# Kernel tuning notes

Measured on AMD Instinct MI355X. Metric: run time of the kernel, lower is better.

The kernel has to match this reference:

```python
import jax, jax.numpy as jnp
import numpy as np

B, N, QD, D, S, H, K = 4, 1024, 320, 512, 1024, 8, 32
DH = D // H  # 64
EPS = 1e-5


def setup_inputs() -> dict:
    key = jax.random.key(0)
    ks = jax.random.split(key, 10)
    sc = 1.0 / np.sqrt(D)
    return {
        "query_states": jax.random.normal(ks[0], (B, N, QD), dtype=jnp.float32),
        "Wqp": jax.random.normal(ks[1], (D, QD), dtype=jnp.float32) / np.sqrt(QD),
        "mem_keys": jax.random.normal(ks[2], (S, D), dtype=jnp.float32),
        "mem_values": jax.random.normal(ks[3], (S, D), dtype=jnp.float32) * 0.1,
        "Wq": jax.random.normal(ks[4], (D, D), dtype=jnp.float32) * sc,
        "Wk": jax.random.normal(ks[5], (D, D), dtype=jnp.float32) * sc,
        "Wv": jax.random.normal(ks[6], (D, D), dtype=jnp.float32) * sc,
        "Wo": jax.random.normal(ks[7], (D, D), dtype=jnp.float32) * sc,
        "ln_g": jnp.ones((D,), dtype=jnp.float32),
        "ln_b": jnp.zeros((D,), dtype=jnp.float32),
        "Wout": jax.random.normal(ks[8], (QD, D), dtype=jnp.float32) * sc,
        "bout": jnp.zeros((QD,), dtype=jnp.float32),
    }


def _l2norm(x):
    return x / jnp.sqrt(jnp.sum(x * x, axis=-1, keepdims=True) + 1e-12)


def reference(query_states, Wqp, mem_keys, mem_values, Wq, Wk, Wv, Wo, ln_g, ln_b, Wout, bout):
    # project queries into memory space: [B,N,D]
    q = jnp.einsum("bnq,dq->bnd", query_states, Wqp)
    # normalize memory slots (normalize_slots=True)
    keys = _l2norm(mem_keys)    # [S,D]
    vals = _l2norm(mem_values)  # [S,D]
    # top-k memory-slot preselection over raw query-key scores
    scores = jnp.einsum("bnd,sd->bns", q, keys)          # [B,N,S]
    _, top_idx = jax.lax.top_k(scores, K)                  # [B,N,K]
    sel_k = jnp.take(keys, top_idx, axis=0)                # [B,N,K,D]
    sel_v = jnp.take(vals, top_idx, axis=0)                # [B,N,K,D]
    # multi-head cross-attention over gathered slots
    qh = jnp.einsum("bnd,ed->bne", q, Wq).reshape(B, N, H, DH)
    kh = jnp.einsum("bnkd,ed->bnke", sel_k, Wk).reshape(B, N, K, H, DH)
    vh = jnp.einsum("bnkd,ed->bnke", sel_v, Wv).reshape(B, N, K, H, DH)
    att = jnp.einsum("bnhd,bnkhd->bnhk", qh, kh) / jnp.sqrt(jnp.float32(DH))  # temperature=1.0
    w = jax.nn.softmax(att, axis=-1)                       # [B,N,H,K]
    ctx = jnp.einsum("bnhk,bnkhd->bnhd", w, vh).reshape(B, N, D)
    ctx = jnp.einsum("bnd,ed->bne", ctx, Wo)               # [B,N,D]
    # output projector: LayerNorm + Linear(memory_dim -> query_dim); dropout inactive (eval)
    mu = jnp.mean(ctx, axis=-1, keepdims=True)
    var = jnp.mean((ctx - mu) ** 2, axis=-1, keepdims=True)
    normed = (ctx - mu) / jnp.sqrt(var + EPS) * ln_g + ln_b
    out = jnp.einsum("bnd,qd->bnq", normed, Wout) + bout   # [B,N,QD]
    return out
```

## Files before the change

kernel.cpp:

```cpp
#include <hip/hip_runtime.h>


__device__ __forceinline__ float bf2f(unsigned short u) {
    return __uint_as_float(((unsigned int)u) << 16);
}
__device__ __forceinline__ unsigned short f2bf(float f) {
    unsigned int u = __float_as_uint(f);
    u += 0x7FFFu + ((u >> 16) & 1u);
    return (unsigned short)(u >> 16);
}
__device__ __forceinline__ int detect_bf(const void* g) {
    return ((*(const unsigned int*)g) & 0xFFFFu) != 0u;
}
__device__ __forceinline__ float ldg1(const void* p, size_t i, int bf) {
    return bf ? bf2f(((const unsigned short*)p)[i]) : ((const float*)p)[i];
}
__device__ __forceinline__ void ld4(const void* p, size_t i, int bf, float* o) {
    if (bf) {
        ushort4 v = *reinterpret_cast<const ushort4*>((const unsigned short*)p + i);
        o[0] = bf2f(v.x); o[1] = bf2f(v.y); o[2] = bf2f(v.z); o[3] = bf2f(v.w);
    } else {
        float4 v = *reinterpret_cast<const float4*>((const float*)p + i);
        o[0] = v.x; o[1] = v.y; o[2] = v.z; o[3] = v.w;
    }
}
__device__ __forceinline__ unsigned int fkey(float x) {
    unsigned int u = __float_as_uint(x);
    return (u & 0x80000000u) ? ~u : (u | 0x80000000u);
}
__device__ __forceinline__ float funkey(unsigned int k) {
    unsigned int u = (k & 0x80000000u) ? (k & 0x7FFFFFFFu) : ~k;
    return __uint_as_float(u);
}

typedef __attribute__((ext_vector_type(8))) short bf16x8;
typedef __attribute__((ext_vector_type(4))) float f32x4;
typedef __attribute__((ext_vector_type(4))) unsigned int u32x4;

__device__ __forceinline__ void split8(const float* x, u32x4& h, u32x4& l) {
#pragma unroll
    for (int j = 0; j < 4; j++) {
        float x0 = x[2 * j], x1 = x[2 * j + 1];
        unsigned int hp, lp;
        asm("v_cvt_pk_bf16_f32 %0, %1, %2" : "=v"(hp) : "v"(x0), "v"(x1));
        float h0 = __uint_as_float(hp << 16);
        float h1 = __uint_as_float(hp & 0xFFFF0000u);
        float l0 = x0 - h0, l1 = x1 - h1;
        asm("v_cvt_pk_bf16_f32 %0, %1, %2" : "=v"(lp) : "v"(l0), "v"(l1));
        h[j] = hp; l[j] = lp;
    }
}

__global__ __launch_bounds__(256) void norms_kernel(
    const void* __restrict__ keys, const void* __restrict__ vals,
    const void* __restrict__ gdet,
    float* __restrict__ inv_kf, float* __restrict__ inv_vf)
{
    __shared__ double red[256];
    int bf = detect_bf(gdet);
    int r = blockIdx.x, t = threadIdx.x;
    const void* src = (r < 1024) ? keys : vals;
    size_t base = (size_t)((r < 1024) ? r : r - 1024) * 512;
    float x0 = ldg1(src, base + t, bf), x1 = ldg1(src, base + t + 256, bf);
    red[t] = (double)x0 * x0 + (double)x1 * x1;
    __syncthreads();
    for (int s = 128; s > 0; s >>= 1) {
        if (t < s) red[t] += red[t + s];
        __syncthreads();
    }
    if (t == 0) {
        float rs = (float)(1.0 / sqrt(red[0] + 1e-12));
        if (r < 1024) inv_kf[r] = rs;
        else          inv_vf[r - 1024] = rs;
    }
}

__global__ __launch_bounds__(256) void transpose_wqp(
    const void* __restrict__ Wqp, const void* __restrict__ gdet,
    float* __restrict__ WqpT)
{
    __shared__ float tile[32][36];
    const int bf = detect_bf(gdet);
    const int t = threadIdx.x;
    const int d0 = blockIdx.x * 32, q0 = blockIdx.y * 32;
    const int r = t >> 3, c = (t & 7) * 4;
    float v[4];
    ld4(Wqp, (size_t)(d0 + r) * 320 + q0 + c, bf, v);
#pragma unroll
    for (int i = 0; i < 4; i++) tile[r][c + i] = v[i];
    __syncthreads();
    float o[4];
#pragma unroll
    for (int i = 0; i < 4; i++) o[i] = tile[c + i][r];
    *reinterpret_cast<float4*>(&WqpT[(size_t)(q0 + r) * 512 + d0 + c]) =
        make_float4(o[0], o[1], o[2], o[3]);
}

__global__ __launch_bounds__(256) void mfma_abt(
    const void* __restrict__ A, const void* __restrict__ B,
    const float* __restrict__ scale, float* __restrict__ C,
    const void* __restrict__ A2, const void* __restrict__ B2,
    const float* __restrict__ scale2, float* __restrict__ C2, int ysplit,
    const float2* __restrict__ stats, const void* __restrict__ g,
    const void* __restrict__ bvec, const void* __restrict__ bias,
    void* __restrict__ O,
    int N, int amode, int abfon, int bbfon, int epi, int npass,
    const void* __restrict__ gdet)
{
    __shared__ __align__(16) short lds[16384];
    const int AHo = 0, ALo = 4096, BHo = 8192, BLo = 12288;
    const int flag = detect_bf(gdet);
    const int abf = abfon ? flag : 0;
    const int bbf = bbfon ? flag : 0;
    const int t = threadIdx.x;
    int by = blockIdx.y;
    const void* Ap = A; const void* Bp = B;
    const float* scp = scale; float* Cp = C;
    if (ysplit && by >= ysplit) { Ap = A2; Bp = B2; scp = scale2; Cp = C2; by -= ysplit; }
    const int m0 = by * 64, n0 = blockIdx.x * 64;
    const int lane = t & 63, wv = t >> 6;
    const int wm = wv >> 1, wn = wv & 1;
    const int srow = t >> 3;
    const int sc8  = t & 7;

    int aoff[2][2], boff[2][2];
#pragma unroll
    for (int mi = 0; mi < 2; mi++)
#pragma unroll
        for (int kk = 0; kk < 2; kk++) {
            int ra = wm * 32 + mi * 16 + (lane & 15);
            int ca = kk * 4 + (lane >> 4);
            aoff[mi][kk] = ra * 64 + ((ca ^ (ra & 7)) << 3);
        }
#pragma unroll
    for (int ni = 0; ni < 2; ni++)
#pragma unroll
        for (int kk = 0; kk < 2; kk++) {
            int rb = wn * 32 + ni * 16 + (lane & 15);
            int cb = kk * 4 + (lane >> 4);
            boff[ni][kk] = rb * 64 + ((cb ^ (rb & 7)) << 3);
        }

    const int addr0 = srow * 64 + ((sc8 ^ (srow & 7)) << 3);
    const int addr1 = addr0 + 32 * 64;

    f32x4 acc[2][2];
#pragma unroll
    for (int mi = 0; mi < 2; mi++)
#pragma unroll
        for (int ni = 0; ni < 2; ni++)
            acc[mi][ni] = (f32x4){0.f, 0.f, 0.f, 0.f};

    for (int ks = 0; ks < 8; ks++) {
        const int kb = ks * 64;
        float av0[8], av1[8], bv0[8], bv1[8];
        ld4(Ap, (size_t)(m0 + srow) * 512 + kb + sc8 * 8,          abf, av0);
        ld4(Ap, (size_t)(m0 + srow) * 512 + kb + sc8 * 8 + 4,      abf, av0 + 4);
        ld4(Ap, (size_t)(m0 + srow + 32) * 512 + kb + sc8 * 8,     abf, av1);
        ld4(Ap, (size_t)(m0 + srow + 32) * 512 + kb + sc8 * 8 + 4, abf, av1 + 4);
        ld4(Bp, (size_t)(n0 + srow) * 512 + kb + sc8 * 8,          bbf, bv0);
        ld4(Bp, (size_t)(n0 + srow) * 512 + kb + sc8 * 8 + 4,      bbf, bv0 + 4);
        ld4(Bp, (size_t)(n0 + srow + 32) * 512 + kb + sc8 * 8,     bbf, bv1);
        ld4(Bp, (size_t)(n0 + srow + 32) * 512 + kb + sc8 * 8 + 4, bbf, bv1 + 4);
        if (amode == 1) {
            float s0 = scp ? scp[m0 + srow] : 1.0f;
            float s1 = scp ? scp[m0 + srow + 32] : 1.0f;
#pragma unroll
            for (int j = 0; j < 8; j++) { av0[j] *= s0; av1[j] *= s1; }
        } else if (amode == 2) {
            float2 st0 = stats[m0 + srow], st1 = stats[m0 + srow + 32];
            float gv[8], bv8[8];
            ld4(g,    (size_t)(kb + sc8 * 8),     flag, gv);
            ld4(g,    (size_t)(kb + sc8 * 8 + 4), flag, gv + 4);
            ld4(bvec, (size_t)(kb + sc8 * 8),     flag, bv8);
            ld4(bvec, (size_t)(kb + sc8 * 8 + 4), flag, bv8 + 4);
#pragma unroll
            for (int j = 0; j < 8; j++) {
                av0[j] = (av0[j] - st0.x) * st0.y * gv[j] + bv8[j];
                av1[j] = (av1[j] - st1.x) * st1.y * gv[j] + bv8[j];
            }
        }
        u32x4 ah0, al0, ah1, al1, bh0, bl0, bh1, bl1;
        split8(av0, ah0, al0); split8(av1, ah1, al1);
        split8(bv0, bh0, bl0); split8(bv1, bh1, bl1);
        __syncthreads();
        *reinterpret_cast<u32x4*>(&lds[AHo + addr0]) = ah0;
        *reinterpret_cast<u32x4*>(&lds[AHo + addr1]) = ah1;
        *reinterpret_cast<u32x4*>(&lds[ALo + addr0]) = al0;
        *reinterpret_cast<u32x4*>(&lds[ALo + addr1]) = al1;
        *reinterpret_cast<u32x4*>(&lds[BHo + addr0]) = bh0;
        *reinterpret_cast<u32x4*>(&lds[BHo + addr1]) = bh1;
        *reinterpret_cast<u32x4*>(&lds[BLo + addr0]) = bl0;
        *reinterpret_cast<u32x4*>(&lds[BLo + addr1]) = bl1;
        __syncthreads();
        for (int p = 0; p < npass; p++) {
            const int Ab = (p == 1 || p == 3) ? ALo : AHo;
            const int Bb = (p >= 2) ? BLo : BHo;
#pragma unroll
            for (int kk = 0; kk < 2; kk++) {
                bf16x8 af[2], bfr[2];
#pragma unroll
                for (int mi = 0; mi < 2; mi++)
                    af[mi] = *reinterpret_cast<const bf16x8*>(&lds[Ab + aoff[mi][kk]]);
#pragma unroll
                for (int ni = 0; ni < 2; ni++)
                    bfr[ni] = *reinterpret_cast<const bf16x8*>(&lds[Bb + boff[ni][kk]]);
#pragma unroll
                for (int mi = 0; mi < 2; mi++)
#pragma unroll
                    for (int ni = 0; ni < 2; ni++)
                        acc[mi][ni] = __builtin_amdgcn_mfma_f32_16x16x32_bf16(
                            af[mi], bfr[ni], acc[mi][ni], 0, 0, 0);
            }
        }
    }

#pragma unroll
    for (int mi = 0; mi < 2; mi++) {
        int mbase = m0 + wm * 32 + mi * 16 + (lane >> 4) * 4;
#pragma unroll
        for (int ni = 0; ni < 2; ni++) {
            int n = n0 + wn * 32 + ni * 16 + (lane & 15);
            if (epi == 0) {
#pragma unroll
                for (int r = 0; r < 4; r++)
                    Cp[(size_t)(mbase + r) * N + n] = acc[mi][ni][r];
            } else {
                float bo = bias ? ldg1(bias, n, flag) : 0.f;
#pragma unroll
                for (int r = 0; r < 4; r++) {
                    float v = acc[mi][ni][r] + bo;
                    size_t off = (size_t)(mbase + r) * N + n;
                    if (flag) ((unsigned short*)O)[off] = f2bf(v);
                    else      ((float*)O)[off] = v;
                }
            }
        }
    }
}

__global__ __launch_bounds__(256) void gemm_scqh(
    const void* __restrict__ X, const float* __restrict__ KWf,
    const float* __restrict__ Mf, const void* __restrict__ gdet,
    float* __restrict__ Sc, float* __restrict__ qh)
{
    __shared__ __align__(16) short lds[24576];
    const int AHo = 0, ALo = 8192, BHo = 16384, BLo = 20480;
    const int bf = detect_bf(gdet);
    const int t = threadIdx.x;
    const int m0 = blockIdx.y * 128, n0 = blockIdx.x * 64;
    const int lane = t & 63, wv = t >> 6;
    const int wm = wv >> 1, wn = wv & 1;
    const int srow = t >> 3;
    const int sc8  = t & 7;

    const float* Wsrc = (n0 < 1024) ? (KWf + (size_t)n0 * 320)
                                    : (Mf + (size_t)(n0 - 1024) * 320);

    int aoff[4][2], boff[2][2];
#pragma unroll
    for (int mi = 0; mi < 4; mi++)
#pragma unroll
        for (int kk = 0; kk < 2; kk++) {
            int ra = wm * 64 + mi * 16 + (lane & 15);
            int ca = kk * 4 + (lane >> 4);
            aoff[mi][kk] = ra * 64 + ((ca ^ (ra & 7)) << 3);
        }
#pragma unroll
    for (int ni = 0; ni < 2; ni++)
#pragma unroll
        for (int kk = 0; kk < 2; kk++) {
            int rb = wn * 32 + ni * 16 + (lane & 15);
            int cb = kk * 4 + (lane >> 4);
            boff[ni][kk] = rb * 64 + ((cb ^ (rb & 7)) << 3);
        }

    f32x4 acc[4][2];
#pragma unroll
    for (int mi = 0; mi < 4; mi++)
#pragma unroll
        for (int ni = 0; ni < 2; ni++)
            acc[mi][ni] = (f32x4){0.f, 0.f, 0.f, 0.f};

    for (int ks = 0; ks < 5; ks++) {
        const int kb = ks * 64;
        u32x4 ah[4], al[4], bh2[2], bl2[2];
#pragma unroll
        for (int i = 0; i < 4; i++) {
            int row = 32 * i + srow;
            float xv[8];
            ld4(X, (size_t)(m0 + row) * 320 + kb + sc8 * 8,     bf, xv);
            ld4(X, (size_t)(m0 + row) * 320 + kb + sc8 * 8 + 4, bf, xv + 4);
            split8(xv, ah[i], al[i]);
        }
#pragma unroll
        for (int i = 0; i < 2; i++) {
            int row = 32 * i + srow;
            const float* s = Wsrc + (size_t)row * 320 + kb + sc8 * 8;
            float4 v0 = *reinterpret_cast<const float4*>(s);
            float4 v1 = *reinterpret_cast<const float4*>(s + 4);
            float xv[8] = {v0.x, v0.y, v0.z, v0.w, v1.x, v1.y, v1.z, v1.w};
            split8(xv, bh2[i], bl2[i]);
        }
        __syncthreads();
#pragma unroll
        for (int i = 0; i < 4; i++) {
            int row = 32 * i + srow;
            int addr = row * 64 + ((sc8 ^ (row & 7)) << 3);
            *reinterpret_cast<u32x4*>(&lds[AHo + addr]) = ah[i];
            *reinterpret_cast<u32x4*>(&lds[ALo + addr]) = al[i];
        }
#pragma unroll
        for (int i = 0; i < 2; i++) {
            int row = 32 * i + srow;
            int addr = row * 64 + ((sc8 ^ (row & 7)) << 3);
            *reinterpret_cast<u32x4*>(&lds[BHo + addr]) = bh2[i];
            *reinterpret_cast<u32x4*>(&lds[BLo + addr]) = bl2[i];
        }
        __syncthreads();
#pragma unroll
        for (int p = 0; p < 3; p++) {
            const int Ab = (p == 1) ? ALo : AHo;
            const int Bb = (p == 2) ? BLo : BHo;
#pragma unroll
            for (int kk = 0; kk < 2; kk++) {
                bf16x8 af[4], bfr[2];
#pragma unroll
                for (int mi = 0; mi < 4; mi++)
                    af[mi] = *reinterpret_cast<const bf16x8*>(&lds[Ab + aoff[mi][kk]]);
#pragma unroll
                for (int ni = 0; ni < 2; ni++)
                    bfr[ni] = *reinterpret_cast<const bf16x8*>(&lds[Bb + boff[ni][kk]]);
#pragma unroll
                for (int mi = 0; mi < 4; mi++)
#pragma unroll
                    for (int ni = 0; ni < 2; ni++)
                        acc[mi][ni] = __builtin_amdgcn_mfma_f32_16x16x32_bf16(
                            af[mi], bfr[ni], acc[mi][ni], 0, 0, 0);
            }
        }
    }

#pragma unroll
    for (int mi = 0; mi < 4; mi++) {
        int mbase = m0 + wm * 64 + mi * 16 + (lane >> 4) * 4;
#pragma unroll
        for (int ni = 0; ni < 2; ni++) {
            int n = n0 + wn * 32 + ni * 16 + (lane & 15);
#pragma unroll
            for (int r = 0; r < 4; r++) {
                float v = acc[mi][ni][r];
                int m = mbase + r;
                if (n0 < 1024) Sc[(size_t)m * 1024 + n] = v;
                else           qh[(size_t)m * 512 + (n - 1024)] = v;
            }
        }
    }
}

__global__ __launch_bounds__(256) void topk_select(
    const float* __restrict__ Sc, const void* __restrict__ X,
    const void* __restrict__ gdet, const float* __restrict__ KWf,
    int* __restrict__ idx)
{
    __shared__ unsigned int srow[4][1024];
    __shared__ unsigned int scv[4][64];
    __shared__ int          sci[4][64];
    const int bf = detect_bf(gdet);
    const int w = threadIdx.x >> 6, lane = threadIdx.x & 63;
    const int row = blockIdx.x * 4 + w;
    const float* S = Sc + (size_t)row * 1024;

#pragma unroll
    for (int q = 0; q < 4; q++) {
        float4 v = *reinterpret_cast<const float4*>(&S[lane * 4 + q * 256]);
        uint4 k = make_uint4(fkey(v.x), fkey(v.y), fkey(v.z), fkey(v.w));
        *reinterpret_cast<uint4*>(&srow[w][lane * 4 + q * 256]) = k;
    }
    scv[w][lane] = 0u;
    sci[w][lane] = 0x7FFFFFFF;
    __syncthreads();

    unsigned int lo = 0u, hi = 0xFFFFFFFFu;
    int cnt_lo = 1024;
    while (cnt_lo > 48 && hi - lo > 1u) {
        unsigned int mid = lo + ((hi - lo) >> 1);
        int c = 0;
#pragma unroll
        for (int q = 0; q < 4; q++) {
            uint4 k = *reinterpret_cast<const uint4*>(&srow[w][lane * 4 + q * 256]);
            c += (k.x >= mid) + (k.y >= mid) + (k.z >= mid) + (k.w >= mid);
        }
#pragma unroll
        for (int o = 1; o < 64; o <<= 1) c += __shfl_xor(c, o, 64);
        if (c >= 33) { lo = mid; cnt_lo = c; }
        else hi = mid;
    }
    const unsigned int T = lo;

    int cl = 0;
#pragma unroll
    for (int q = 0; q < 4; q++) {
        uint4 k = *reinterpret_cast<const uint4*>(&srow[w][lane * 4 + q * 256]);
        cl += (k.x >= T) + (k.y >= T) + (k.z >= T) + (k.w >= T);
    }
    int inc = cl;
#pragma unroll
    for (int o = 1; o < 64; o <<= 1) {
        int y = __shfl_up(inc, o, 64);
        if (lane >= o) inc += y;
    }
    int pos = inc - cl;
#pragma unroll
    for (int q = 0; q < 4; q++) {
        uint4 k = *reinterpret_cast<const uint4*>(&srow[w][lane * 4 + q * 256]);
        int base = lane * 4 + q * 256;
        if (k.x >= T && pos < 64) { scv[w][pos] = k.x; sci[w][pos] = base + 0; pos++; }
        if (k.y >= T && pos < 64) { scv[w][pos] = k.y; sci[w][pos] = base + 1; pos++; }
        if (k.z >= T && pos < 64) { scv[w][pos] = k.z; sci[w][pos] = base + 2; pos++; }
        if (k.w >= T && pos < 64) { scv[w][pos] = k.w; sci[w][pos] = base + 3; pos++; }
    }
    __syncthreads();
    unsigned int cv = scv[w][lane];
    int          ci = sci[w][lane];
#pragma unroll
    for (int k = 2; k <= 64; k <<= 1) {
#pragma unroll
        for (int jj = k >> 1; jj > 0; jj >>= 1) {
            unsigned int ov = __shfl_xor(cv, jj, 64);
            int          oi = __shfl_xor(ci, jj, 64);
            bool up = ((lane & k) == 0);
            bool takemax = (((lane & jj) == 0) == up);
            bool othergreater = (ov > cv) || (ov == cv && oi < ci);
            if (takemax == othergreater) { cv = ov; ci = oi; }
        }
    }
    float v31 = funkey(__shfl(cv, 31, 64));
    float v32 = funkey(__shfl(cv, 32, 64));
    if (v31 - v32 > 2.5e-4f) {
        if (lane < 32) idx[(size_t)row * 32 + lane] = ci;
        return;
    }
    size_t xb = (size_t)row * 320;
    bool active = (lane < 48) && (ci != 0x7FFFFFFF);
    int cidx = active ? ci : 0x7FFFFFFF;
    const float* kr = KWf + (size_t)(active ? ci : 0) * 320;
    double s = 0.0;
#pragma unroll 4
    for (int d = 0; d < 320; d++) {
        float xd = ldg1(X, xb + d, bf);
        s += (double)xd * (double)kr[d];
    }
    if (!active) s = -1.0e300;
#pragma unroll
    for (int k = 2; k <= 64; k <<= 1) {
#pragma unroll
        for (int jj = k >> 1; jj > 0; jj >>= 1) {
            double os = __shfl_xor(s, jj, 64);
            int    oi = __shfl_xor(cidx, jj, 64);
            bool up = ((lane & k) == 0);
            bool takemax = (((lane & jj) == 0) == up);
            bool og = (os > s) || (os == s && oi < cidx);
            if (takemax == og) { s = os; cidx = oi; }
        }
    }
    if (lane < 32) idx[(size_t)row * 32 + lane] = cidx;
}

__global__ __launch_bounds__(256) void attn_kernel(
    const float* __restrict__ qh, const float* __restrict__ Kp,
    const float* __restrict__ Vp, const int* __restrict__ idx,
    float* __restrict__ ctx)
{
    __shared__ float sq[512];
    __shared__ int   sidx[32];
    __shared__ float sl[8][32];
    __shared__ float sw[8][32];
    int row = blockIdx.x, t = threadIdx.x;
    int w = t >> 6, l = t & 63;
    if (t < 128)
        *reinterpret_cast<float4*>(&sq[t * 4]) =
            *reinterpret_cast<const float4*>(&qh[(size_t)row * 512 + t * 4]);
    if (t < 32) {
        int v = idx[(size_t)row * 32 + t];
        sidx[t] = (v < 0) ? 0 : (v > 1023 ? 1023 : v);
    }
    __syncthreads();

    float4 q0 = *reinterpret_cast<const float4*>(&sq[l * 8]);
    float4 q1 = *reinterpret_cast<const float4*>(&sq[l * 8 + 4]);
    int h = l >> 3;
#pragma unroll
    for (int i = 0; i < 8; i++) {
        int s = w * 8 + i;
        const float* kp = Kp + (size_t)sidx[s] * 512 + l * 8;
        float4 k0 = *reinterpret_cast<const float4*>(kp);
        float4 k1 = *reinterpret_cast<const float4*>(kp + 4);
        float p = q0.x * k0.x + q0.y * k0.y + q0.z * k0.z + q0.w * k0.w
                + q1.x * k1.x + q1.y * k1.y + q1.z * k1.z + q1.w * k1.w;
        p += __shfl_xor(p, 1, 64);
        p += __shfl_xor(p, 2, 64);
        p += __shfl_xor(p, 4, 64);
        if ((l & 7) == 0) sl[h][s] = p * 0.125f;
    }
    __syncthreads();

    int hh = t >> 5, kk = t & 31;
    float logit = sl[hh][kk];
    float m = -1e30f;
#pragma unroll
    for (int i = 0; i < 32; i++) m = fmaxf(m, sl[hh][i]);
    float ssum = 0.f;
#pragma unroll
    for (int i = 0; i < 32; i++) ssum += __expf(sl[hh][i] - m);
    sw[hh][kk] = __expf(logit - m) / ssum;
    __syncthreads();

    int c = t * 2, hc = c >> 6;
    float ax = 0.f, ay = 0.f;
#pragma unroll
    for (int k2 = 0; k2 < 32; k2++) {
        float2 vv = *reinterpret_cast<const float2*>(&Vp[(size_t)sidx[k2] * 512 + c]);
        float wgt = sw[hc][k2];
        ax += wgt * vv.x; ay += wgt * vv.y;
    }
    *reinterpret_cast<float2*>(&ctx[(size_t)row * 512 + c]) = make_float2(ax, ay);
}

__global__ __launch_bounds__(256) void ln_stats(
    const float* __restrict__ co, float2* __restrict__ stats)
{
    int w = threadIdx.x >> 6, lane = threadIdx.x & 63;
    int row = blockIdx.x * 4 + w;
    const float* p = co + (size_t)row * 512;
    float4 a = *reinterpret_cast<const float4*>(&p[lane * 8]);
    float4 b = *reinterpret_cast<const float4*>(&p[lane * 8 + 4]);
    double s  = (double)a.x + (double)a.y + (double)a.z + (double)a.w
              + (double)b.x + (double)b.y + (double)b.z + (double)b.w;
    double ss = (double)a.x * a.x + (double)a.y * a.y + (double)a.z * a.z
              + (double)a.w * a.w + (double)b.x * b.x + (double)b.y * b.y
              + (double)b.z * b.z + (double)b.w * b.w;
#pragma unroll
    for (int o = 1; o < 64; o <<= 1) {
        s  += __shfl_xor(s, o, 64);
        ss += __shfl_xor(ss, o, 64);
    }
    if (lane == 0) {
        double mu = s / 512.0, var = ss / 512.0 - mu * mu;
        stats[row] = make_float2((float)mu, (float)(1.0 / sqrt(var + 1e-5)));
    }
}

extern "C" void kernel_launch(void* const* d_in, const int* in_sizes, int n_in,
                              void* d_out, int out_size, void* d_ws, size_t ws_size,
                              hipStream_t stream)
{
    const void* X    = d_in[0];
    const void* Wqp  = d_in[1];
    const void* keys = d_in[2];
    const void* vals = d_in[3];
    const void* Wq   = d_in[4];
    const void* Wk   = d_in[5];
    const void* Wv   = d_in[6];
    const void* Wo   = d_in[7];
    const void* ln_g = d_in[8];
    const void* ln_b = d_in[9];
    const void* Wout = d_in[10];
    const void* bout = d_in[11];

    float* ws = (float*)d_ws;
    float*  Sc     = ws;
    float*  co     = ws;
    float*  Yreg   = ws + 2097152;
    float*  qh     = ws + 4194304;
    float*  Mf     = ws + 6291456;
    float*  Kp     = ws + 6291456;
    float*  KWf    = ws + 6815744;
    float*  Vp     = ws + 6815744;
    float*  WqpT   = ws + 7340032;
    int*    idx    = (int*)(ws + 7995392);
    float*  inv_kf = ws + 8128512;
    float*  inv_vf = ws + 8129536;
    float*  ctx    = Yreg;
    float2* stats  = (float2*)Yreg;

    norms_kernel<<<2048, 256, 0, stream>>>(keys, vals, ln_g, inv_kf, inv_vf);
    transpose_wqp<<<dim3(16, 10), 256, 0, stream>>>(Wqp, ln_g, WqpT);
    mfma_abt<<<dim3(5, 24), 256, 0, stream>>>(
        keys, WqpT, inv_kf, KWf, Wq, WqpT, nullptr, Mf, 16,
        nullptr, nullptr, nullptr, nullptr, nullptr,
        320, 1, 1, 0, 0, 4, ln_g);
    gemm_scqh<<<dim3(24, 32), 256, 0, stream>>>(X, KWf, Mf, ln_g, Sc, qh);
    topk_select<<<1024, 256, 0, stream>>>(Sc, X, ln_g, KWf, idx);
    mfma_abt<<<dim3(8, 32), 256, 0, stream>>>(
        keys, Wk, inv_kf, Kp, vals, Wv, inv_vf, Vp, 16,
        nullptr, nullptr, nullptr, nullptr, nullptr,
        512, 1, 1, 1, 0, 3, ln_g);
    attn_kernel<<<4096, 256, 0, stream>>>(qh, Kp, Vp, idx, ctx);
    mfma_abt<<<dim3(8, 64), 256, 0, stream>>>(
        ctx, Wo, nullptr, co, nullptr, nullptr, nullptr, nullptr, 0,
        nullptr, nullptr, nullptr, nullptr, nullptr,
        512, 0, 0, 1, 0, 3, ln_g);
    ln_stats<<<1024, 256, 0, stream>>>(co, stats);
    mfma_abt<<<dim3(5, 64), 256, 0, stream>>>(
        co, Wout, nullptr, nullptr, nullptr, nullptr, nullptr, nullptr, 0,
        stats, ln_g, ln_b, bout, d_out,
        320, 2, 0, 1, 1, 3, ln_g);
}
```

Before: 245.2 us.

## Pre-split GEMM operands into bf16 hi/lo and stream via global_load_lds

Adds a presplit kernel that converts the query states into bf16 high/low halves once, and makes the weight-fusion GEMM emit bf16 hi/lo copies of its outputs in its epilogue. The score/qh GEMM then loads these pre-split operands directly into LDS with global_load_lds (swizzled), so it no longer converts in registers or does the register-to-LDS store. This removes per-tile split work and register staging, in exchange for an extra kernel launch, extra workspace traffic for the hi/lo buffers, and narrow scalar 16-bit stores in the epilogue.

New measurement: 245.0 us. No clear change (-0.1%).

```diff
diff --git a/kernel.cpp b/kernel.cpp
--- a/kernel.cpp
+++ b/kernel.cpp
@@ -49,6 +49,13 @@
         asm("v_cvt_pk_bf16_f32 %0, %1, %2" : "=v"(lp) : "v"(l0), "v"(l1));
         h[j] = hp; l[j] = lp;
     }
+}
+
+__device__ __forceinline__ void gload16(const void* g, void* l) {
+    __builtin_amdgcn_global_load_lds(
+        (const __attribute__((address_space(1))) unsigned int*)g,
+        (__attribute__((address_space(3))) unsigned int*)l,
+        16, 0, 0);
 }
 
 __global__ __launch_bounds__(256) void norms_kernel(
@@ -96,6 +103,22 @@
         make_float4(o[0], o[1], o[2], o[3]);
 }
 
+__global__ __launch_bounds__(256) void presplit(
+    const void* __restrict__ src, const void* __restrict__ gdet,
+    unsigned short* __restrict__ H, unsigned short* __restrict__ L, int total8)
+{
+    int i = blockIdx.x * 256 + threadIdx.x;
+    if (i >= total8) return;
+    int bf = detect_bf(gdet);
+    float v[8];
+    ld4(src, (size_t)i * 8, bf, v);
+    ld4(src, (size_t)i * 8 + 4, bf, v + 4);
+    u32x4 h, l;
+    split8(v, h, l);
+    *reinterpret_cast<u32x4*>(H + (size_t)i * 8) = h;
+    *reinterpret_cast<u32x4*>(L + (size_t)i * 8) = l;
+}
+
 __global__ __launch_bounds__(256) void mfma_abt(
     const void* __restrict__ A, const void* __restrict__ B,
     const float* __restrict__ scale, float* __restrict__ C,
@@ -104,6 +127,8 @@
     const float2* __restrict__ stats, const void* __restrict__ g,
     const void* __restrict__ bvec, const void* __restrict__ bias,
     void* __restrict__ O,
+    unsigned short* __restrict__ Hout, unsigned short* __restrict__ Lout,
+    int hrow0a, int hrow0b,
     int N, int amode, int abfon, int bbfon, int epi, int npass,
     const void* __restrict__ gdet)
 {
@@ -116,7 +141,10 @@
     int by = blockIdx.y;
     const void* Ap = A; const void* Bp = B;
     const float* scp = scale; float* Cp = C;
-    if (ysplit && by >= ysplit) { Ap = A2; Bp = B2; scp = scale2; Cp = C2; by -= ysplit; }
+    int hrow0 = hrow0a;
+    if (ysplit && by >= ysplit) {
+        Ap = A2; Bp = B2; scp = scale2; Cp = C2; by -= ysplit; hrow0 = hrow0b;
+    }
     const int m0 = by * 64, n0 = blockIdx.x * 64;
     const int lane = t & 63, wv = t >> 6;
     const int wm = wv >> 1, wn = wv & 1;
@@ -223,8 +251,17 @@
             int n = n0 + wn * 32 + ni * 16 + (lane & 15);
             if (epi == 0) {
 #pragma unroll
-                for (int r = 0; r < 4; r++)
-                    Cp[(size_t)(mbase + r) * N + n] = acc[mi][ni][r];
+                for (int r = 0; r < 4; r++) {
+                    float v = acc[mi][ni][r];
+                    Cp[(size_t)(mbase + r) * N + n] = v;
+                    if (Hout) {
+                        unsigned short hb = f2bf(v);
+                        unsigned short lb = f2bf(v - bf2f(hb));
+                        size_t ho = (size_t)(hrow0 + mbase + r) * N + n;
+                        Hout[ho] = hb;
+                        Lout[ho] = lb;
+                    }
+                }
             } else {
                 float bo = bias ? ldg1(bias, n, flag) : 0.f;
 #pragma unroll
@@ -240,22 +277,18 @@
 }
 
 __global__ __launch_bounds__(256) void gemm_scqh(
-    const void* __restrict__ X, const float* __restrict__ KWf,
-    const float* __restrict__ Mf, const void* __restrict__ gdet,
+    const unsigned short* __restrict__ Xh, const unsigned short* __restrict__ Xl,
+    const unsigned short* __restrict__ Bh, const unsigned short* __restrict__ Bl,
     float* __restrict__ Sc, float* __restrict__ qh)
 {
     __shared__ __align__(16) short lds[24576];
     const int AHo = 0, ALo = 8192, BHo = 16384, BLo = 20480;
-    const int bf = detect_bf(gdet);
     const int t = threadIdx.x;
     const int m0 = blockIdx.y * 128, n0 = blockIdx.x * 64;
     const int lane = t & 63, wv = t >> 6;
     const int wm = wv >> 1, wn = wv & 1;
-    const int srow = t >> 3;
-    const int sc8  = t & 7;
-
-    const float* Wsrc = (n0 < 1024) ? (KWf + (size_t)n0 * 320)
-                                    : (Mf + (size_t)(n0 - 1024) * 320);
+    const int lr = lane >> 3;
+    const int lc = lane & 7;
 
     int aoff[4][2], boff[2][2];
 #pragma unroll
@@ -282,40 +315,28 @@
         for (int ni = 0; ni < 2; ni++)
             acc[mi][ni] = (f32x4){0.f, 0.f, 0.f, 0.f};
 
+    char* smem = (char*)lds;
+
     for (int ks = 0; ks < 5; ks++) {
         const int kb = ks * 64;
-        u32x4 ah[4], al[4], bh2[2], bl2[2];
+        __syncthreads();
 #pragma unroll
         for (int i = 0; i < 4; i++) {
-            int row = 32 * i + srow;
-            float xv[8];
-            ld4(X, (size_t)(m0 + row) * 320 + kb + sc8 * 8,     bf, xv);
-            ld4(X, (size_t)(m0 + row) * 320 + kb + sc8 * 8 + 4, bf, xv + 4);
-            split8(xv, ah[i], al[i]);
+            int r0 = wv * 32 + i * 8;
+            int r  = r0 + lr;
+            int sc = lc ^ (r & 7);
+            size_t go = (size_t)(m0 + r) * 320 + kb + sc * 8;
+            gload16(Xh + go, smem + (AHo << 1) + r0 * 128);
+            gload16(Xl + go, smem + (ALo << 1) + r0 * 128);
         }
 #pragma unroll
         for (int i = 0; i < 2; i++) {
-            int row = 32 * i + srow;
-            const float* s = Wsrc + (size_t)row * 320 + kb + sc8 * 8;
-            float4 v0 = *reinterpret_cast<const float4*>(s);
-            float4 v1 = *reinterpret_cast<const float4*>(s + 4);
-            float xv[8] = {v0.x, v0.y, v0.z, v0.w, v1.x, v1.y, v1.z, v1.w};
-            split8(xv, bh2[i], bl2[i]);
-        }
-        __syncthreads();
-#pragma unroll
-        for (int i = 0; i < 4; i++) {
-            int row = 32 * i + srow;
-            int addr = row * 64 + ((sc8 ^ (row & 7)) << 3);
-            *reinterpret_cast<u32x4*>(&lds[AHo + addr]) = ah[i];
-            *reinterpret_cast<u32x4*>(&lds[ALo + addr]) = al[i];
-        }
-#pragma unroll
-        for (int i = 0; i < 2; i++) {
-            int row = 32 * i + srow;
-            int addr = row * 64 + ((sc8 ^ (row & 7)) << 3);
-            *reinterpret_cast<u32x4*>(&lds[BHo + addr]) = bh2[i];
-            *reinterpret_cast<u32x4*>(&lds[BLo + addr]) = bl2[i];
+            int r0 = wv * 16 + i * 8;
+            int r  = r0 + lr;
+            int sc = lc ^ (r & 7);
+            size_t go = (size_t)(n0 + r) * 320 + kb + sc * 8;
+            gload16(Bh + go, smem + (BHo << 1) + r0 * 128);
+            gload16(Bl + go, smem + (BLo << 1) + r0 * 128);
         }
         __syncthreads();
 #pragma unroll
@@ -581,29 +602,38 @@
     int*    idx    = (int*)(ws + 7995392);
     float*  inv_kf = ws + 8128512;
     float*  inv_vf = ws + 8129536;
+    unsigned short* Xh  = (unsigned short*)(ws + 8388608);
+    unsigned short* Xl  = (unsigned short*)(ws + 9043968);
+    unsigned short* Bh  = (unsigned short*)(ws + 9699328);
+    unsigned short* Bl  = (unsigned short*)(ws + 9945088);
     float*  ctx    = Yreg;
     float2* stats  = (float2*)Yreg;
 
     norms_kernel<<<2048, 256, 0, stream>>>(keys, vals, ln_g, inv_kf, inv_vf);
     transpose_wqp<<<dim3(16, 10), 256, 0, stream>>>(Wqp, ln_g, WqpT);
+    presplit<<<640, 256, 0, stream>>>(X, ln_g, Xh, Xl, 163840);
     mfma_abt<<<dim3(5, 24), 256, 0, stream>>>(
         keys, WqpT, inv_kf, KWf, Wq, WqpT, nullptr, Mf, 16,
         nullptr, nullptr, nullptr, nullptr, nullptr,
+        Bh, Bl, 0, 1024,
         320, 1, 1, 0, 0, 4, ln_g);
-    gemm_scqh<<<dim3(24, 32), 256, 0, stream>>>(X, KWf, Mf, ln_g, Sc, qh);
+    gemm_scqh<<<dim3(24, 32), 256, 0, stream>>>(Xh, Xl, Bh, Bl, Sc, qh);
     topk_select<<<1024, 256, 0, stream>>>(Sc, X, ln_g, KWf, idx);
     mfma_abt<<<dim3(8, 32), 256, 0, stream>>>(
         keys, Wk, inv_kf, Kp, vals, Wv, inv_vf, Vp, 16,
         nullptr, nullptr, nullptr, nullptr, nullptr,
+        nullptr, nullptr, 0, 0,
         512, 1, 1, 1, 0, 3, ln_g);
     attn_kernel<<<4096, 256, 0, stream>>>(qh, Kp, Vp, idx, ctx);
     mfma_abt<<<dim3(8, 64), 256, 0, stream>>>(
         ctx, Wo, nullptr, co, nullptr, nullptr, nullptr, nullptr, 0,
         nullptr, nullptr, nullptr, nullptr, nullptr,
+        nullptr, nullptr, 0, 0,
         512, 0, 0, 1, 0, 3, ln_g);
     ln_stats<<<1024, 256, 0, stream>>>(co, stats);
     mfma_abt<<<dim3(5, 64), 256, 0, stream>>>(
         co, Wout, nullptr, nullptr, nullptr, nullptr, nullptr, nullptr, 0,
         stats, ln_g, ln_b, bout, d_out,
+        nullptr, nullptr, 0, 0,
         320, 2, 0, 1, 1, 3, ln_g);
 }
```
